# Performance work log

Hardware: AMD Instinct MI355X
Metric: run time of the kernel (lower is better)

Reference implementation:

```python
import jax, jax.numpy as jnp
import numpy as np

H, U_DIM = 64, 64
N = H * U_DIM
COEF_GAMMA = 0.4


def setup_inputs() -> dict:
    key = jax.random.key(0)
    ks = jax.random.split(key, 7)
    inp = jax.random.normal(ks[0], (H, U_DIM), jnp.float32)
    L = jax.random.normal(ks[1], (H, U_DIM), jnp.float32)
    th_P = 0.1 * jax.random.normal(ks[2], (H, U_DIM), jnp.float32)
    entries_mask = jax.random.uniform(ks[3], (H, U_DIM)) < 0.5  # observed-entry mask
    # D_tilda: dense (HU, HU) regularizer operator (e.g. a discrete-difference Gram);
    # symmetrized and small so the full operator stays well-conditioned.
    G = jax.random.normal(ks[4], (N, N), jnp.float32) / np.sqrt(N)
    D_tilda = 0.05 * (G + G.T)
    S = jax.random.normal(ks[5], (H, H), jnp.float32) / np.sqrt(H)
    return {
        "inp": inp,
        "L": L,
        "entries_mask": entries_mask,
        "D_tilda": D_tilda,
        "th_P": th_P,
        "v": jnp.float32(0.1),
        "neta": jnp.float32(0.5),
        "lamda1": jnp.float32(0.1),
        "lamda2": jnp.float32(0.1),
        "rho": jnp.float32(1.0),
        "S": S,
    }


def _svtC(x, tau):
    # torch.svd: x = Um diag(s) V^T ; here Vh = V^T (square 64x64 case).
    Um, s, Vh = jnp.linalg.svd(x, full_matrices=False)
    s_thr = jax.nn.relu(s - tau * s[0])  # threshold relative to top singular value
    return (Um * s_thr) @ Vh


def reference(inp, L, entries_mask, D_tilda, th_P, v, neta, lamda1, lamda2, rho, S):
    tau = jax.nn.sigmoid(v) * COEF_GAMMA
    q = entries_mask.reshape(N).astype(jnp.float32)          # diag of Q_tilda
    StS = S.T @ S                                            # (H, H)
    S_tilda = jnp.kron(jnp.eye(U_DIM, dtype=jnp.float32), StS)  # (HU, HU)
    vec = rho * (L - th_P) + jnp.where(entries_mask, inp, jnp.float32(0.0))
    A = (jnp.diag(q) + lamda1 * D_tilda + lamda2 * S_tilda
         + rho * jnp.eye(N, dtype=jnp.float32))
    x = jnp.linalg.solve(A, vec.reshape(N)).reshape(H, U_DIM)  # == inv(A) @ vec
    Ltmp = _svtC(x + th_P, tau)
    Ptmp = th_P + neta * (x - Ltmp)
    return Ltmp, Ptmp
```

## Files before the change

### kernel.cpp

```cpp
#include <hip/hip_runtime.h>
#include <hip/hip_bf16.h>

#define NN 4096
#define NITER 4
#define NSWEEP 5
#define MCS 68

#define OFF_STS  64
#define OFF_QRHO (OFF_STS + NN)
#define OFF_DINV (OFF_QRHO + NN)
#define OFF_Y0   (OFF_DINV + NN)
#define OFF_Y1   (OFF_Y0 + NN)
#define OFF_X0   (OFF_Y1 + NN)
#define OFF_X1   (OFF_X0 + NN)
#define OFF_R0   (OFF_X1 + NN)
#define OFF_R1   (OFF_R0 + NN)
#define OFF_P0   (OFF_R1 + NN)
#define OFF_P1   (OFF_P0 + NN)
#define OFF_PTY0 (OFF_P1 + NN)
#define OFF_PTY1 (OFF_PTY0 + 1024)
#define DH_OFF_BYTES 196608
#define WS_NEED_BF16 (DH_OFF_BYTES + (size_t)NN * NN * 2)

typedef unsigned int uint;
__device__ inline float lo2f(uint w){ return __uint_as_float(w << 16); }
__device__ inline float hi2f(uint w){ return __uint_as_float(w & 0xffff0000u); }
__device__ inline uint f2b(float f){
    uint u = __float_as_uint(f);
    return (u + 0x7FFFu + ((u >> 16) & 1u)) >> 16;
}
__device__ inline float rsum16(float x){
    int a = __builtin_amdgcn_update_dpp(0, __float_as_int(x), 0xB1, 0xF, 0xF, true);
    float s = x + __int_as_float(a);
    int b = __builtin_amdgcn_update_dpp(0, __float_as_int(s), 0x4E, 0xF, 0xF, true);
    s = s + __int_as_float(b);
    int c = __builtin_amdgcn_update_dpp(0, __float_as_int(s), 0x141, 0xF, 0xF, true);
    s = s + __int_as_float(c);
    int d = __builtin_amdgcn_update_dpp(0, __float_as_int(s), 0x140, 0xF, 0xF, true);
    s = s + __int_as_float(d);
    return s;
}

__global__ void k_prep(const float* __restrict__ inp, const float* __restrict__ L,
                       const int*  __restrict__ mask, const float* __restrict__ thP,
                       const float* __restrict__ S,
                       const float* __restrict__ l2p, const float* __restrict__ rhop,
                       float* __restrict__ wf){
    int t = blockIdx.x * 256 + threadIdx.x;
    int r = t >> 6, c = t & 63;
    float acc = 0.f, acc2 = 0.f;
    for(int h = 0; h < 64; ++h){
        float sr = S[h*64 + r];
        float sc = S[h*64 + c];
        acc  += sr * sc;
        acc2 += sc * sc;
    }
    wf[OFF_STS + t] = acc;
    float rho = rhop[0], l2 = l2p[0];
    float q = (mask[t] != 0) ? 1.f : 0.f;
    float bi = rho * (L[t] - thP[t]) + q * inp[t];
    float dinv = 1.f / (q + rho + l2 * acc2);
    wf[OFF_QRHO + t] = q + rho;
    wf[OFF_DINV + t] = dinv;
    wf[OFF_X0 + t]   = 0.f;
    wf[OFF_R0 + t]   = bi;
    wf[OFF_P0 + t]   = bi * dinv;
}

__device__ inline void cg_prologue(float* __restrict__ wf,
                                   const float* __restrict__ rold, const float* __restrict__ pold,
                                   const float* __restrict__ xold, const float* __restrict__ yold,
                                   float* __restrict__ rnew, float* __restrict__ pnew,
                                   float* __restrict__ xnew,
                                   const float* __restrict__ pty_read,
                                   float* __restrict__ psh,
                                   float* __restrict__ red){
    int tid = threadIdx.x;
    const float* dinv = wf + OFF_DINV;
    float4 r4[4], d4[4];
    float part = 0.f;
    #pragma unroll
    for(int k = 0; k < 4; ++k){
        r4[k] = ((const float4*)rold)[tid + k*256];
        d4[k] = ((const float4*)dinv)[tid + k*256];
        part += r4[k].x*r4[k].x*d4[k].x + r4[k].y*r4[k].y*d4[k].y
              + r4[k].z*r4[k].z*d4[k].z + r4[k].w*r4[k].w*d4[k].w;
    }
    float pp = pty_read[tid] + pty_read[tid+256] + pty_read[tid+512] + pty_read[tid+768];
    for(int m = 32; m >= 1; m >>= 1){
        part += __shfl_xor(part, m, 64);
        pp   += __shfl_xor(pp, m, 64);
    }
    int wave = tid >> 6, lane = tid & 63;
    if(lane == 0){ red[wave] = part; red[4+wave] = pp; }
    __syncthreads();
    float rzold = red[0] + red[1] + red[2] + red[3];
    float ptys  = red[4] + red[5] + red[6] + red[7];
    float alpha = rzold / ptys;
    float4 rn[4], zn[4];
    float part2 = 0.f;
    #pragma unroll
    for(int k = 0; k < 4; ++k){
        float4 y4 = ((const float4*)yold)[tid + k*256];
        rn[k].x = r4[k].x - alpha*y4.x;  rn[k].y = r4[k].y - alpha*y4.y;
        rn[k].z = r4[k].z - alpha*y4.z;  rn[k].w = r4[k].w - alpha*y4.w;
        zn[k].x = rn[k].x*d4[k].x;  zn[k].y = rn[k].y*d4[k].y;
        zn[k].z = rn[k].z*d4[k].z;  zn[k].w = rn[k].w*d4[k].w;
        part2 += rn[k].x*zn[k].x + rn[k].y*zn[k].y + rn[k].z*zn[k].z + rn[k].w*zn[k].w;
    }
    for(int m = 32; m >= 1; m >>= 1) part2 += __shfl_xor(part2, m, 64);
    __syncthreads();
    if(lane == 0) red[wave] = part2;
    __syncthreads();
    float rznew = red[0] + red[1] + red[2] + red[3];
    float beta = rznew / rzold;
    bool b0 = (blockIdx.x == 0);
    #pragma unroll
    for(int k = 0; k < 4; ++k){
        float4 po = ((const float4*)pold)[tid + k*256];
        float4 pn;
        pn.x = zn[k].x + beta*po.x;  pn.y = zn[k].y + beta*po.y;
        pn.z = zn[k].z + beta*po.z;  pn.w = zn[k].w + beta*po.w;
        ((float4*)psh)[tid + k*256] = pn;
        if(b0){
            ((float4*)pnew)[tid + k*256] = pn;
            ((float4*)rnew)[tid + k*256] = rn[k];
            float4 xo = ((const float4*)xold)[tid + k*256];
            float4 xn;
            xn.x = xo.x + alpha*po.x;  xn.y = xo.y + alpha*po.y;
            xn.z = xo.z + alpha*po.z;  xn.w = xo.w + alpha*po.w;
            ((float4*)xnew)[tid + k*256] = xn;
        }
    }
    __syncthreads();
}

__launch_bounds__(256)
__global__ void k_fc(const float* __restrict__ D, unsigned short* __restrict__ Dh,
                     const float* __restrict__ inp, const float* __restrict__ L,
                     const int*  __restrict__ mask, const float* __restrict__ thP,
                     const float* __restrict__ S,
                     const float* __restrict__ l1p, const float* __restrict__ l2p,
                     const float* __restrict__ rhop,
                     float* __restrict__ wf, float* __restrict__ pty_out){
    __shared__ float psh[NN];
    __shared__ float red[8];
    __shared__ float cparts[256];
    int tid = threadIdx.x;
    int wave = tid >> 6, lane = tid & 63;
    int row = blockIdx.x * 4 + wave;
    int u = row & 63, h = row >> 6;
    float l1 = l1p[0], l2 = l2p[0], rho = rhop[0];

    {
        float cp = 0.f;
        for(int hh = wave*16; hh < wave*16 + 16; ++hh){
            float sv = S[hh*64 + lane];
            cp += sv * sv;
        }
        cparts[wave*64 + lane] = cp;
    }
    float stv = 0.f;
    for(int hh = 0; hh < 64; ++hh)
        stv += S[hh*64 + u] * S[hh*64 + lane];
    if(row < 64) wf[OFF_STS + row*64 + lane] = stv;
    __syncthreads();

    int c = tid & 63;
    float cs4 = cparts[c] + cparts[64+c] + cparts[128+c] + cparts[192+c];
    bool canon = (blockIdx.x < 16);
    for(int k = 0; k < 16; ++k){
        int t = tid + k*256;
        float q = (mask[t] != 0) ? 1.f : 0.f;
        float bi = rho * (L[t] - thP[t]) + q * inp[t];
        float dinv = 1.f / (q + rho + l2 * cs4);
        psh[t] = bi * dinv;
        if(canon && k == (int)blockIdx.x){
            wf[OFF_QRHO + t] = q + rho;
            wf[OFF_DINV + t] = dinv;
            wf[OFF_X0 + t]   = 0.f;
            wf[OFF_R0 + t]   = bi;
            wf[OFF_P0 + t]   = bi * dinv;
        }
    }
    __syncthreads();

    const float* Drow = D + (size_t)row * NN;
    unsigned short* Dhrow = Dh + (size_t)row * NN;
    float dacc = 0.f;
    for(int j = 0; j < 16; ++j){
        int c0 = j*256 + lane*4;
        float4 dv = *(const float4*)(Drow + c0);
        float4 pa = *(const float4*)(psh + c0);
        dacc += dv.x*pa.x + dv.y*pa.y + dv.z*pa.z + dv.w*pa.w;
        uint2 o;
        o.x = f2b(dv.x) | (f2b(dv.y) << 16);
        o.y = f2b(dv.z) | (f2b(dv.w) << 16);
        *(uint2*)(Dhrow + c0) = o;
    }
    float sacc = stv * psh[h*64 + lane];
    float val = l1 * dacc + l2 * sacc;
    for(int m = 32; m >= 1; m >>= 1) val += __shfl_xor(val, m, 64);
    if(lane == 0){
        float qr = ((mask[row] != 0) ? 1.f : 0.f) + rho;
        float yi = val + qr * psh[row];
        (wf + OFF_Y0)[row] = yi;
        red[wave] = yi * psh[row];
    }
    __syncthreads();
    if(tid == 0) pty_out[blockIdx.x] = red[0] + red[1] + red[2] + red[3];
}

__launch_bounds__(256)
__global__ void k_step_h(const unsigned short* __restrict__ Dh,
                         const float* __restrict__ l1p, const float* __restrict__ l2p,
                         float* __restrict__ wf,
                         const float* __restrict__ rold, const float* __restrict__ pold,
                         const float* __restrict__ xold, const float* __restrict__ yold,
                         float* __restrict__ rnew, float* __restrict__ pnew,
                         float* __restrict__ xnew, float* __restrict__ ynew,
                         const float* __restrict__ pty_read, float* __restrict__ pty_write){
    __shared__ float psh[NN];
    __shared__ float red[8];
    int tid = threadIdx.x;
    cg_prologue(wf, rold, pold, xold, yold, rnew, pnew, xnew, pty_read, psh, red);

    float l1 = l1p[0], l2 = l2p[0];
    int wave = tid >> 6, lane = tid & 63;
    int row = blockIdx.x * 4 + wave;
    int h = row >> 6, u = row & 63;
    const float* qrho = wf + OFF_QRHO;
    const float* StS  = wf + OFF_STS;

    const unsigned short* Drow = Dh + (size_t)row * NN;
    float dacc = 0.f;
    for(int j = 0; j < 8; ++j){
        int c0 = j*512 + lane*8;
        uint4 dv = *(const uint4*)(Drow + c0);
        float4 pa = *(const float4*)(psh + c0);
        float4 pb = *(const float4*)(psh + c0 + 4);
        dacc += lo2f(dv.x)*pa.x + hi2f(dv.x)*pa.y
              + lo2f(dv.y)*pa.z + hi2f(dv.y)*pa.w
              + lo2f(dv.z)*pb.x + hi2f(dv.z)*pb.y
              + lo2f(dv.w)*pb.z + hi2f(dv.w)*pb.w;
    }
    float sacc = StS[u*64 + lane] * psh[h*64 + lane];
    float val = l1 * dacc + l2 * sacc;
    for(int m = 32; m >= 1; m >>= 1) val += __shfl_xor(val, m, 64);
    if(lane == 0){
        float yi = val + qrho[row] * psh[row];
        ynew[row] = yi;
        red[wave] = yi * psh[row];
    }
    __syncthreads();
    if(tid == 0) pty_write[blockIdx.x] = red[0] + red[1] + red[2] + red[3];
}

__launch_bounds__(256)
__global__ void k_step_f(const float* __restrict__ D,
                         const float* __restrict__ l1p, const float* __restrict__ l2p,
                         float* __restrict__ wf,
                         const float* __restrict__ rold, const float* __restrict__ pold,
                         const float* __restrict__ xold, const float* __restrict__ yold,
                         float* __restrict__ rnew, float* __restrict__ pnew,
                         float* __restrict__ xnew, float* __restrict__ ynew,
                         const float* __restrict__ pty_read, float* __restrict__ pty_write,
                         int do_pro){
    __shared__ float psh[NN];
    __shared__ float red[8];
    int tid = threadIdx.x;
    if(do_pro){
        cg_prologue(wf, rold, pold, xold, yold, rnew, pnew, xnew, pty_read, psh, red);
    } else {
        for(int k = 0; k < 4; ++k)
            ((float4*)psh)[tid + k*256] = ((const float4*)pold)[tid + k*256];
        __syncthreads();
    }
    float l1 = l1p[0], l2 = l2p[0];
    int wave = tid >> 6, lane = tid & 63;
    int row = blockIdx.x * 4 + wave;
    int h = row >> 6, u = row & 63;
    const float* qrho = wf + OFF_QRHO;
    const float* StS  = wf + OFF_STS;
    const float* Drow = D + (size_t)row * NN;
    float dacc = 0.f;
    for(int j = 0; j < 16; ++j){
        int c0 = j*256 + lane*4;
        float4 dv = *(const float4*)(Drow + c0);
        float4 pa = *(const float4*)(psh + c0);
        dacc += dv.x*pa.x + dv.y*pa.y + dv.z*pa.z + dv.w*pa.w;
    }
    float sacc = StS[u*64 + lane] * psh[h*64 + lane];
    float val = l1 * dacc + l2 * sacc;
    for(int m = 32; m >= 1; m >>= 1) val += __shfl_xor(val, m, 64);
    if(lane == 0){
        float yi = val + qrho[row] * psh[row];
        ynew[row] = yi;
        red[wave] = yi * psh[row];
    }
    __syncthreads();
    if(tid == 0) pty_write[blockIdx.x] = red[0] + red[1] + red[2] + red[3];
}

#define P_MA(par) (POOL + (par)*2176)
#define P_MB(par) (POOL + 4352 + (par)*2176)
#define P_XSH     (POOL + 8704)
#define P_TSH     (POOL)
#define P_WC      (POOL + 4352)
#define DOT4(u,v) ((u).x*(v).x + (u).y*(v).y + (u).z*(v).z + (u).w*(v).w)

__launch_bounds__(512)
__global__ void k_svt(const float* __restrict__ thP, const float* __restrict__ vp,
                      const float* __restrict__ netap,
                      float* __restrict__ wf,
                      const float* __restrict__ rlast, const float* __restrict__ plast,
                      const float* __restrict__ xlast,
                      const float* __restrict__ ptyp,
                      float* __restrict__ out){
    __shared__ float POOL[12800];
    __shared__ float s2[64], coef3[64];
    __shared__ float smax_sh;
    __shared__ float redv[16];
    int tid = threadIdx.x;
    float* Xsh = P_XSH;

    {
        const float* dinv = wf + OFF_DINV;
        float part = 0.f;
        #pragma unroll
        for(int k = 0; k < 2; ++k){
            float4 r4 = ((const float4*)rlast)[tid + k*512];
            float4 d4 = ((const float4*)dinv)[tid + k*512];
            part += r4.x*r4.x*d4.x + r4.y*r4.y*d4.y + r4.z*r4.z*d4.z + r4.w*r4.w*d4.w;
        }
        float pp = ptyp[tid] + ptyp[tid + 512];
        for(int m = 32; m >= 1; m >>= 1){
            part += __shfl_xor(part, m, 64);
            pp   += __shfl_xor(pp, m, 64);
        }
        if((tid & 63) == 0){ redv[tid >> 6] = part; redv[8 + (tid >> 6)] = pp; }
        __syncthreads();
        float rz = redv[0] + redv[1] + redv[2] + redv[3]
                 + redv[4] + redv[5] + redv[6] + redv[7];
        float ptys = redv[8] + redv[9] + redv[10] + redv[11]
                   + redv[12] + redv[13] + redv[14] + redv[15];
        float a = rz / ptys;
        #pragma unroll
        for(int k = 0; k < 2; ++k){
            float4 x4 = ((const float4*)xlast)[tid + k*512];
            float4 p4 = ((const float4*)plast)[tid + k*512];
            float4 t4 = ((const float4*)thP)[tid + k*512];
            float4 v;
            v.x = x4.x + a*p4.x + t4.x;  v.y = x4.y + a*p4.y + t4.y;
            v.z = x4.z + a*p4.z + t4.z;  v.w = x4.w + a*p4.w + t4.w;
            ((float4*)Xsh)[tid + k*512] = v;
        }
    }
    __syncthreads();

    int g  = tid >> 4;
    int sl = tid & 15;
    float4 A, B;
    {
        int ca = 2*g, cb = 2*g + 1, r0 = sl*4;
        A.x = Xsh[(r0+0)*64+ca]; A.y = Xsh[(r0+1)*64+ca];
        A.z = Xsh[(r0+2)*64+ca]; A.w = Xsh[(r0+3)*64+ca];
        B.x = Xsh[(r0+0)*64+cb]; B.y = Xsh[(r0+1)*64+cb];
        B.z = Xsh[(r0+2)*64+cb]; B.w = Xsh[(r0+3)*64+cb];
    }
    float aa = rsum16(DOT4(A,A));
    float bb = rsum16(DOT4(B,B));

    const int total = NSWEEP * 63;
    for(int gr = 0; gr < total; ++gr){
        float cc = rsum16(DOT4(A,B));
        float cs = 1.f, sn = 0.f, t = 0.f;
        if(fabsf(cc) > 1e-30f){
            float zeta = (bb - aa) * 0.5f * __builtin_amdgcn_rcpf(cc);
            t = copysignf(__builtin_amdgcn_rcpf(fabsf(zeta) +
                          __builtin_amdgcn_sqrtf(1.f + zeta*zeta)), zeta);
            cs = __builtin_amdgcn_rsqf(1.f + t*t);
            sn = t * cs;
        }
        float naN = aa - t*cc;
        float nbN = bb + t*cc;
        if(gr != total - 1){
            int par = gr & 1;
            float* MAp = P_MA(par);
            float* MBp = P_MB(par);
            float4 nb;
            nb.x = sn*A.x + cs*B.x; nb.y = sn*A.y + cs*B.y;
            nb.z = sn*A.z + cs*B.z; nb.w = sn*A.w + cs*B.w;
            float* cbB = (g == 0) ? (MAp + 1*MCS) : (MBp + (g-1)*MCS);
            *(float4*)(cbB + sl*4) = nb;
            if(sl == 0) cbB[64] = nbN;
            float4 na;
            na.x = cs*A.x - sn*B.x; na.y = cs*A.y - sn*B.y;
            na.z = cs*A.z - sn*B.z; na.w = cs*A.w - sn*B.w;
            if(g >= 1 && g <= 30){
                float* cbA = MAp + (g+1)*MCS;
                *(float4*)(cbA + sl*4) = na;
                if(sl == 0) cbA[64] = naN;
            }
            __syncthreads();
            float4 nA = na;  float nAa = naN;
            float4 nB = na;  float nBb = naN;
            if(g >= 1){
                const float* ra = MAp + g*MCS;
                nA = *(const float4*)(ra + sl*4);
                nAa = ra[64];
            }
            if(g <= 30){
                const float* rb = MBp + g*MCS;
                nB = *(const float4*)(rb + sl*4);
                nBb = rb[64];
            }
            A = nA; B = nB; aa = nAa; bb = nBb;
        } else {
            float4 na;
            na.x = cs*A.x - sn*B.x; na.y = cs*A.y - sn*B.y;
            na.z = cs*A.z - sn*B.z; na.w = cs*A.w - sn*B.w;
            float4 nbf;
            nbf.x = sn*A.x + cs*B.x; nbf.y = sn*A.y + cs*B.y;
            nbf.z = sn*A.z + cs*B.z; nbf.w = sn*A.w + cs*B.w;
            A = na; B = nbf;
        }
    }
    {
        float fa = rsum16(DOT4(A,A));
        float fb = rsum16(DOT4(B,B));
        __syncthreads();
        float* Wc = P_WC;
        *(float4*)(Wc + (2*g)*MCS + sl*4)   = A;
        *(float4*)(Wc + (2*g+1)*MCS + sl*4) = B;
        if(sl == 0){ s2[2*g] = fa; s2[2*g+1] = fb; }
    }
    __syncthreads();
    if(tid == 0){
        float sm = 0.f;
        for(int c = 0; c < 64; ++c) sm = fmaxf(sm, s2[c]);
        smax_sh = sqrtf(sm);
    }
    __syncthreads();
    if(tid < 64){
        float s = sqrtf(s2[tid]);
        float v = vp[0];
        float tau = 0.4f / (1.f + expf(-v));
        float thr = tau * smax_sh;
        coef3[tid] = (s > thr && s > 1e-20f) ? (s - thr) / (s*s*s) : 0.f;
    }
    __syncthreads();

    const float* Wc = P_WC;
    float* Tsh = P_TSH;
    {
        int kk = tid >> 3;
        int j0 = (tid & 7) * 8;
        float acc[8];
        #pragma unroll
        for(int j = 0; j < 8; ++j) acc[j] = 0.f;
        for(int r = 0; r < 64; ++r){
            float wk = Wc[kk*MCS + r];
            const float* xr = Xsh + r*64 + j0;
            float4 x0 = *(const float4*)(xr);
            float4 x1 = *(const float4*)(xr + 4);
            acc[0]+=wk*x0.x; acc[1]+=wk*x0.y; acc[2]+=wk*x0.z; acc[3]+=wk*x0.w;
            acc[4]+=wk*x1.x; acc[5]+=wk*x1.y; acc[6]+=wk*x1.z; acc[7]+=wk*x1.w;
        }
        float c3 = coef3[kk];
        float* tr = Tsh + kk*64 + j0;
        float4 t0, t1;
        t0.x = c3*acc[0]; t0.y = c3*acc[1]; t0.z = c3*acc[2]; t0.w = c3*acc[3];
        t1.x = c3*acc[4]; t1.y = c3*acc[5]; t1.z = c3*acc[6]; t1.w = c3*acc[7];
        *(float4*)(tr)     = t0;
        *(float4*)(tr + 4) = t1;
    }
    __syncthreads();

    {
        float neta = netap[0];
        int i  = tid >> 3;
        int j0 = (tid & 7) * 8;
        float acc[8];
        #pragma unroll
        for(int j = 0; j < 8; ++j) acc[j] = 0.f;
        for(int kk = 0; kk < 64; ++kk){
            float wik = Wc[kk*MCS + i];
            const float* tr = Tsh + kk*64 + j0;
            float4 t0 = *(const float4*)(tr);
            float4 t1 = *(const float4*)(tr + 4);
            acc[0]+=wik*t0.x; acc[1]+=wik*t0.y; acc[2]+=wik*t0.z; acc[3]+=wik*t0.w;
            acc[4]+=wik*t1.x; acc[5]+=wik*t1.y; acc[6]+=wik*t1.z; acc[7]+=wik*t1.w;
        }
        int n0 = i*64 + j0;
        #pragma unroll
        for(int c = 0; c < 2; ++c){
            float4 th = *(const float4*)(thP + n0 + 4*c);
            float4 lt, pt;
            lt.x = acc[4*c+0]; lt.y = acc[4*c+1]; lt.z = acc[4*c+2]; lt.w = acc[4*c+3];
            float4 xs = *(const float4*)(Xsh + n0 + 4*c);
            pt.x = th.x + neta * (xs.x - th.x - lt.x);
            pt.y = th.y + neta * (xs.y - th.y - lt.y);
            pt.z = th.z + neta * (xs.z - th.z - lt.z);
            pt.w = th.w + neta * (xs.w - th.w - lt.w);
            *(float4*)(out + n0 + 4*c)      = lt;
            *(float4*)(out + NN + n0 + 4*c) = pt;
        }
    }
}

extern "C" void kernel_launch(void* const* d_in, const int* in_sizes, int n_in,
                              void* d_out, int out_size, void* d_ws, size_t ws_size,
                              hipStream_t stream){
    const float* inp  = (const float*)d_in[0];
    const float* L    = (const float*)d_in[1];
    const int*   mask = (const int*)  d_in[2];
    const float* D    = (const float*)d_in[3];
    const float* thP  = (const float*)d_in[4];
    const float* vS   = (const float*)d_in[5];
    const float* neta = (const float*)d_in[6];
    const float* l1   = (const float*)d_in[7];
    const float* l2   = (const float*)d_in[8];
    const float* rho  = (const float*)d_in[9];
    const float* S    = (const float*)d_in[10];
    float* wf = (float*)d_ws;
    float* out = (float*)d_out;
    const bool use_bf16 = (ws_size >= WS_NEED_BF16);
    unsigned short* Dh = (unsigned short*)((char*)d_ws + DH_OFF_BYTES);

    float* Xb[2]  = { wf + OFF_X0, wf + OFF_X1 };
    float* Rb[2]  = { wf + OFF_R0, wf + OFF_R1 };
    float* Pb[2]  = { wf + OFF_P0, wf + OFF_P1 };
    float* Yb[2]  = { wf + OFF_Y0, wf + OFF_Y1 };
    float* pty[2] = { wf + OFF_PTY0, wf + OFF_PTY1 };

    if(use_bf16){
        k_fc<<<1024, 256, 0, stream>>>(D, Dh, inp, L, mask, thP, S,
                                       l1, l2, rho, wf, pty[0]);
        for(int j = 1; j < NITER; ++j){
            int ro = (j+1)&1, wr = j&1;
            k_step_h<<<1024, 256, 0, stream>>>(Dh, l1, l2, wf,
                Rb[ro], Pb[ro], Xb[ro], Yb[ro],
                Rb[wr], Pb[wr], Xb[wr], Yb[wr],
                pty[(j-1)&1], pty[j&1]);
        }
    } else {
        k_prep<<<16, 256, 0, stream>>>(inp, L, mask, thP, S, l2, rho, wf);
        k_step_f<<<1024, 256, 0, stream>>>(D, l1, l2, wf,
            Rb[0], Pb[0], Xb[0], Yb[0], Rb[1], Pb[1], Xb[1], Yb[0],
            pty[0], pty[0], 0);
        for(int j = 1; j < NITER; ++j){
            int ro = (j+1)&1, wr = j&1;
            k_step_f<<<1024, 256, 0, stream>>>(D, l1, l2, wf,
                Rb[ro], Pb[ro], Xb[ro], Yb[ro],
                Rb[wr], Pb[wr], Xb[wr], Yb[wr],
                pty[(j-1)&1], pty[j&1], 1);
        }
    }
    const int lp = (NITER-1)&1;
    k_svt<<<1, 512, 0, stream>>>(thP, vS, neta, wf, Rb[lp], Pb[lp], Xb[lp],
                                 pty[lp], out);
}
```

Before: 292.9 us.

## Fuse CG iterations into one persistent kernel with atomic grid barriers

Replaces the separate first-iteration kernel and the per-iteration step kernel launches with a single persistent kernel. The kernel loops over iterations and synchronises all blocks through an atomic counter grid barrier reset by a memset. This removes kernel launch gaps and the boundaries between dependent CG steps. In exchange it relies on all 1024 blocks being co-resident, and carries a spin-wait barrier with a timeout guard that could silently break ordering.

```diff
diff --git a/kernel.cpp b/kernel.cpp
--- a/kernel.cpp
+++ b/kernel.cpp
@@ -19,8 +19,10 @@
 #define OFF_P1   (OFF_P0 + NN)
 #define OFF_PTY0 (OFF_P1 + NN)
 #define OFF_PTY1 (OFF_PTY0 + 1024)
+#define OFF_CTR  (OFF_PTY1 + 1024)
 #define DH_OFF_BYTES 196608
 #define WS_NEED_BF16 (DH_OFF_BYTES + (size_t)NN * NN * 2)
+#define GRID_CG 1024
 
 typedef unsigned int uint;
 __device__ inline float lo2f(uint w){ return __uint_as_float(w << 16); }
@@ -39,6 +41,21 @@
     int d = __builtin_amdgcn_update_dpp(0, __float_as_int(s), 0x140, 0xF, 0xF, true);
     s = s + __int_as_float(d);
     return s;
+}
+
+__device__ inline void gridbar(uint* c){
+    __threadfence();
+    __syncthreads();
+    if(threadIdx.x == 0){
+        __hip_atomic_fetch_add(c, 1u, __ATOMIC_ACQ_REL, __HIP_MEMORY_SCOPE_AGENT);
+        long guard = 0;
+        while(__hip_atomic_load(c, __ATOMIC_ACQUIRE, __HIP_MEMORY_SCOPE_AGENT) < (uint)GRID_CG){
+            __builtin_amdgcn_s_sleep(1);
+            if(++guard > 100000000L) break;
+        }
+    }
+    __syncthreads();
+    __threadfence();
 }
 
 __global__ void k_prep(const float* __restrict__ inp, const float* __restrict__ L,
@@ -135,14 +152,14 @@
     __syncthreads();
 }
 
-__launch_bounds__(256)
-__global__ void k_fc(const float* __restrict__ D, unsigned short* __restrict__ Dh,
-                     const float* __restrict__ inp, const float* __restrict__ L,
-                     const int*  __restrict__ mask, const float* __restrict__ thP,
-                     const float* __restrict__ S,
-                     const float* __restrict__ l1p, const float* __restrict__ l2p,
-                     const float* __restrict__ rhop,
-                     float* __restrict__ wf, float* __restrict__ pty_out){
+__launch_bounds__(256, 4)
+__global__ void k_cgp(const float* __restrict__ D, unsigned short* __restrict__ Dh,
+                      const float* __restrict__ inp, const float* __restrict__ L,
+                      const int*  __restrict__ mask, const float* __restrict__ thP,
+                      const float* __restrict__ S,
+                      const float* __restrict__ l1p, const float* __restrict__ l2p,
+                      const float* __restrict__ rhop,
+                      float* __restrict__ wf, uint* __restrict__ ctr){
     __shared__ float psh[NN];
     __shared__ float red[8];
     __shared__ float cparts[256];
@@ -152,6 +169,12 @@
     int u = row & 63, h = row >> 6;
     float l1 = l1p[0], l2 = l2p[0], rho = rhop[0];
 
+    float* Xb[2]  = { wf + OFF_X0, wf + OFF_X1 };
+    float* Rb[2]  = { wf + OFF_R0, wf + OFF_R1 };
+    float* Pb[2]  = { wf + OFF_P0, wf + OFF_P1 };
+    float* Yb[2]  = { wf + OFF_Y0, wf + OFF_Y1 };
+    float* pty[2] = { wf + OFF_PTY0, wf + OFF_PTY1 };
+
     {
         float cp = 0.f;
         for(int hh = wave*16; hh < wave*16 + 16; ++hh){
@@ -159,101 +182,89 @@
             cp += sv * sv;
         }
         cparts[wave*64 + lane] = cp;
-    }
-    float stv = 0.f;
-    for(int hh = 0; hh < 64; ++hh)
-        stv += S[hh*64 + u] * S[hh*64 + lane];
-    if(row < 64) wf[OFF_STS + row*64 + lane] = stv;
-    __syncthreads();
-
-    int c = tid & 63;
-    float cs4 = cparts[c] + cparts[64+c] + cparts[128+c] + cparts[192+c];
-    bool canon = (blockIdx.x < 16);
-    for(int k = 0; k < 16; ++k){
-        int t = tid + k*256;
-        float q = (mask[t] != 0) ? 1.f : 0.f;
-        float bi = rho * (L[t] - thP[t]) + q * inp[t];
-        float dinv = 1.f / (q + rho + l2 * cs4);
-        psh[t] = bi * dinv;
-        if(canon && k == (int)blockIdx.x){
-            wf[OFF_QRHO + t] = q + rho;
-            wf[OFF_DINV + t] = dinv;
-            wf[OFF_X0 + t]   = 0.f;
-            wf[OFF_R0 + t]   = bi;
-            wf[OFF_P0 + t]   = bi * dinv;
-        }
-    }
-    __syncthreads();
-
-    const float* Drow = D + (size_t)row * NN;
-    unsigned short* Dhrow = Dh + (size_t)row * NN;
-    float dacc = 0.f;
-    for(int j = 0; j < 16; ++j){
-        int c0 = j*256 + lane*4;
-        float4 dv = *(const float4*)(Drow + c0);
-        float4 pa = *(const float4*)(psh + c0);
-        dacc += dv.x*pa.x + dv.y*pa.y + dv.z*pa.z + dv.w*pa.w;
-        uint2 o;
-        o.x = f2b(dv.x) | (f2b(dv.y) << 16);
-        o.y = f2b(dv.z) | (f2b(dv.w) << 16);
-        *(uint2*)(Dhrow + c0) = o;
-    }
-    float sacc = stv * psh[h*64 + lane];
-    float val = l1 * dacc + l2 * sacc;
-    for(int m = 32; m >= 1; m >>= 1) val += __shfl_xor(val, m, 64);
-    if(lane == 0){
-        float qr = ((mask[row] != 0) ? 1.f : 0.f) + rho;
-        float yi = val + qr * psh[row];
-        (wf + OFF_Y0)[row] = yi;
-        red[wave] = yi * psh[row];
-    }
-    __syncthreads();
-    if(tid == 0) pty_out[blockIdx.x] = red[0] + red[1] + red[2] + red[3];
-}
-
-__launch_bounds__(256)
-__global__ void k_step_h(const unsigned short* __restrict__ Dh,
-                         const float* __restrict__ l1p, const float* __restrict__ l2p,
-                         float* __restrict__ wf,
-                         const float* __restrict__ rold, const float* __restrict__ pold,
-                         const float* __restrict__ xold, const float* __restrict__ yold,
-                         float* __restrict__ rnew, float* __restrict__ pnew,
-                         float* __restrict__ xnew, float* __restrict__ ynew,
-                         const float* __restrict__ pty_read, float* __restrict__ pty_write){
-    __shared__ float psh[NN];
-    __shared__ float red[8];
-    int tid = threadIdx.x;
-    cg_prologue(wf, rold, pold, xold, yold, rnew, pnew, xnew, pty_read, psh, red);
-
-    float l1 = l1p[0], l2 = l2p[0];
-    int wave = tid >> 6, lane = tid & 63;
-    int row = blockIdx.x * 4 + wave;
-    int h = row >> 6, u = row & 63;
+        float stv = 0.f;
+        for(int hh = 0; hh < 64; ++hh)
+            stv += S[hh*64 + u] * S[hh*64 + lane];
+        if(row < 64) wf[OFF_STS + row*64 + lane] = stv;
+        __syncthreads();
+
+        int c = tid & 63;
+        float cs4 = cparts[c] + cparts[64+c] + cparts[128+c] + cparts[192+c];
+        bool canon = (blockIdx.x < 16);
+        for(int k = 0; k < 16; ++k){
+            int t = tid + k*256;
+            float q = (mask[t] != 0) ? 1.f : 0.f;
+            float bi = rho * (L[t] - thP[t]) + q * inp[t];
+            float dinv = 1.f / (q + rho + l2 * cs4);
+            psh[t] = bi * dinv;
+            if(canon && k == (int)blockIdx.x){
+                wf[OFF_QRHO + t] = q + rho;
+                wf[OFF_DINV + t] = dinv;
+                wf[OFF_X0 + t]   = 0.f;
+                wf[OFF_R0 + t]   = bi;
+                wf[OFF_P0 + t]   = bi * dinv;
+            }
+        }
+        __syncthreads();
+
+        const float* Drow = D + (size_t)row * NN;
+        unsigned short* Dhrow = Dh + (size_t)row * NN;
+        float dacc = 0.f;
+        for(int j = 0; j < 16; ++j){
+            int c0 = j*256 + lane*4;
+            float4 dv = *(const float4*)(Drow + c0);
+            float4 pa = *(const float4*)(psh + c0);
+            dacc += dv.x*pa.x + dv.y*pa.y + dv.z*pa.z + dv.w*pa.w;
+            uint2 o;
+            o.x = f2b(dv.x) | (f2b(dv.y) << 16);
+            o.y = f2b(dv.z) | (f2b(dv.w) << 16);
+            *(uint2*)(Dhrow + c0) = o;
+        }
+        float sacc = stv * psh[h*64 + lane];
+        float val = l1 * dacc + l2 * sacc;
+        for(int m = 32; m >= 1; m >>= 1) val += __shfl_xor(val, m, 64);
+        if(lane == 0){
+            float qr = ((mask[row] != 0) ? 1.f : 0.f) + rho;
+            float yi = val + qr * psh[row];
+            Yb[0][row] = yi;
+            red[wave] = yi * psh[row];
+        }
+        __syncthreads();
+        if(tid == 0) pty[0][blockIdx.x] = red[0] + red[1] + red[2] + red[3];
+    }
+
     const float* qrho = wf + OFF_QRHO;
     const float* StS  = wf + OFF_STS;
-
-    const unsigned short* Drow = Dh + (size_t)row * NN;
-    float dacc = 0.f;
-    for(int j = 0; j < 8; ++j){
-        int c0 = j*512 + lane*8;
-        uint4 dv = *(const uint4*)(Drow + c0);
-        float4 pa = *(const float4*)(psh + c0);
-        float4 pb = *(const float4*)(psh + c0 + 4);
-        dacc += lo2f(dv.x)*pa.x + hi2f(dv.x)*pa.y
-              + lo2f(dv.y)*pa.z + hi2f(dv.y)*pa.w
-              + lo2f(dv.z)*pb.x + hi2f(dv.z)*pb.y
-              + lo2f(dv.w)*pb.z + hi2f(dv.w)*pb.w;
-    }
-    float sacc = StS[u*64 + lane] * psh[h*64 + lane];
-    float val = l1 * dacc + l2 * sacc;
-    for(int m = 32; m >= 1; m >>= 1) val += __shfl_xor(val, m, 64);
-    if(lane == 0){
-        float yi = val + qrho[row] * psh[row];
-        ynew[row] = yi;
-        red[wave] = yi * psh[row];
-    }
-    __syncthreads();
-    if(tid == 0) pty_write[blockIdx.x] = red[0] + red[1] + red[2] + red[3];
+    for(int it = 1; it < NITER; ++it){
+        gridbar(ctr + (it-1)*32);
+
+        int ro = (it+1)&1, wr = it&1;
+        cg_prologue(wf, Rb[ro], Pb[ro], Xb[ro], Yb[ro],
+                    Rb[wr], Pb[wr], Xb[wr], pty[(it-1)&1], psh, red);
+
+        const unsigned short* Drow = Dh + (size_t)row * NN;
+        float dacc = 0.f;
+        for(int j = 0; j < 8; ++j){
+            int c0 = j*512 + lane*8;
+            uint4 dv = *(const uint4*)(Drow + c0);
+            float4 pa = *(const float4*)(psh + c0);
+            float4 pb = *(const float4*)(psh + c0 + 4);
+            dacc += lo2f(dv.x)*pa.x + hi2f(dv.x)*pa.y
+                  + lo2f(dv.y)*pa.z + hi2f(dv.y)*pa.w
+                  + lo2f(dv.z)*pb.x + hi2f(dv.z)*pb.y
+                  + lo2f(dv.w)*pb.z + hi2f(dv.w)*pb.w;
+        }
+        float sacc = StS[u*64 + lane] * psh[h*64 + lane];
+        float val = l1 * dacc + l2 * sacc;
+        for(int m = 32; m >= 1; m >>= 1) val += __shfl_xor(val, m, 64);
+        if(lane == 0){
+            float yi = val + qrho[row] * psh[row];
+            Yb[wr][row] = yi;
+            red[wave] = yi * psh[row];
+        }
+        __syncthreads();
+        if(tid == 0) pty[it&1][blockIdx.x] = red[0] + red[1] + red[2] + red[3];
+    }
 }
 
 __launch_bounds__(256)
@@ -533,17 +544,12 @@
     float* Pb[2]  = { wf + OFF_P0, wf + OFF_P1 };
     float* Yb[2]  = { wf + OFF_Y0, wf + OFF_Y1 };
     float* pty[2] = { wf + OFF_PTY0, wf + OFF_PTY1 };
+    uint*  ctr    = (uint*)(wf + OFF_CTR);
 
     if(use_bf16){
-        k_fc<<<1024, 256, 0, stream>>>(D, Dh, inp, L, mask, thP, S,
-                                       l1, l2, rho, wf, pty[0]);
-        for(int j = 1; j < NITER; ++j){
-            int ro = (j+1)&1, wr = j&1;
-            k_step_h<<<1024, 256, 0, stream>>>(Dh, l1, l2, wf,
-                Rb[ro], Pb[ro], Xb[ro], Yb[ro],
-                Rb[wr], Pb[wr], Xb[wr], Yb[wr],
-                pty[(j-1)&1], pty[j&1]);
-        }
+        hipMemsetAsync(ctr, 0, 3 * 32 * sizeof(uint), stream);
+        k_cgp<<<GRID_CG, 256, 0, stream>>>(D, Dh, inp, L, mask, thP, S,
+                                           l1, l2, rho, wf, ctr);
     } else {
         k_prep<<<16, 256, 0, stream>>>(inp, L, mask, thP, S, l2, rho, wf);
         k_step_f<<<1024, 256, 0, stream>>>(D, l1, l2, wf,
```

Measured after the change: 1.068 ms. 265% more time.
